# Performance work log

Hardware: AMD Instinct MI355X
Metric: run time of the kernel (lower is better)

## Reference

```python
import jax, jax.numpy as jnp
import numpy as np

TOP_K = 2


def setup_inputs() -> dict:
    key = jax.random.key(0)
    ks = jax.random.split(key, 6)
    B, S, D, F, E = 4, 2048, 1024, 4096, 8
    sd = 1.0 / np.sqrt(D)
    sf = 1.0 / np.sqrt(F)
    return {
        "x": jax.random.normal(ks[0], (B, S, D), dtype=jnp.float32),
        "gate_w": jax.random.normal(ks[1], (D, E), dtype=jnp.float32) * sd,
        "w1": jax.random.normal(ks[2], (E, D, F), dtype=jnp.float32) * sd,
        "b1": jax.random.normal(ks[3], (E, F), dtype=jnp.float32) * 0.01,
        "w2": jax.random.normal(ks[4], (E, F, D), dtype=jnp.float32) * sf,
        "b2": jax.random.normal(ks[5], (E, D), dtype=jnp.float32) * 0.01,
    }


def reference(x, gate_w, w1, b1, w2, b2):
    B, S, D = x.shape
    E = gate_w.shape[1]
    xf = x.reshape(-1, D)                        # [T, D], T = B*S
    T = xf.shape[0]

    # Gating: top-k logits, softmax over the selected k (in fp32, as in torch)
    logits = xf @ gate_w                         # [T, E]
    top_vals, top_idx = jax.lax.top_k(logits, TOP_K)            # [T, K]
    wts = jax.nn.softmax(top_vals.astype(jnp.float32), axis=-1).astype(x.dtype)

    # Dense combine weights: combine[t, e] = sum_k wts[t,k] * [top_idx[t,k]==e]
    rows = jnp.arange(T)[:, None]
    combine = jnp.zeros((T, E), dtype=x.dtype).at[rows, top_idx].add(wts)

    # Expert FFNs (dropout is identity in eval; torch GELU default = exact erf)
    out = jnp.zeros_like(xf)
    for e in range(E):
        h = jax.nn.gelu(xf @ w1[e] + b1[e], approximate=False)  # [T, F]
        out = out + combine[:, e:e + 1] * (h @ w2[e] + b2[e])
    return out.reshape(B, S, D)
```

## Files before the change

kernel.cpp:

```cpp
#include <hip/hip_runtime.h>


#define T_TOK 8192
#define D_DIM 1024
#define F_DIM 4096
#define E_NUM 8
#define BM 256
#define BN 256
#define BK 32
#define NK1 (D_DIM / BK)
#define NK2 (F_DIM / BK)
#define NX1 (F_DIM / BN)
#define NX2 (D_DIM / BN)
#define MAX_TILES (T_TOK * 2 / BM + E_NUM)

typedef float f32x4 __attribute__((ext_vector_type(4)));
typedef short bf16x8 __attribute__((ext_vector_type(8)));

__device__ __forceinline__ unsigned short f2bf(float f) {
  union { float f; unsigned u; } v; v.f = f;
  unsigned r = v.u + 0x7FFFu + ((v.u >> 16) & 1u);
  return (unsigned short)(r >> 16);
}

__device__ __forceinline__ void async_cp16(const unsigned short* g, unsigned short* l) {
  __builtin_amdgcn_global_load_lds((__attribute__((address_space(1))) void*)g,
                                   (__attribute__((address_space(3))) void*)l,
                                   16, 0, 0);
}

#define WAIT_VM4 asm volatile("s_waitcnt vmcnt(4)" ::: "memory")
#define WAIT_LGKM0 asm volatile("s_waitcnt lgkmcnt(0)" ::: "memory")
#define RAW_BARRIER asm volatile("s_barrier" ::: "memory")


__global__ void cast_x_kernel(const float* __restrict__ src,
                              unsigned short* __restrict__ dst, int n4) {
  int i = blockIdx.x * blockDim.x + threadIdx.x;
  if (i >= n4) return;
  float4 v = ((const float4*)src)[i];
  ushort4 o;
  o.x = f2bf(v.x); o.y = f2bf(v.y); o.z = f2bf(v.z); o.w = f2bf(v.w);
  ((ushort4*)dst)[i] = o;
}

__global__ __launch_bounds__(256) void transpose_cast_kernel(
    const float* __restrict__ src, unsigned short* __restrict__ dst,
    int R, int C) {
  __shared__ float tile[64][65];
  int e = blockIdx.z;
  src += (size_t)e * R * C;
  dst += (size_t)e * R * C;
  int c0 = blockIdx.x * 64;
  int r0 = blockIdx.y * 64;
  int t = threadIdx.x;
  int cl = (t & 15) * 4, rl = t >> 4;
#pragma unroll
  for (int i = 0; i < 4; ++i) {
    int r = rl + i * 16;
    float4 v = *(const float4*)(src + (size_t)(r0 + r) * C + c0 + cl);
    tile[r][cl + 0] = v.x;
    tile[r][cl + 1] = v.y;
    tile[r][cl + 2] = v.z;
    tile[r][cl + 3] = v.w;
  }
  __syncthreads();
  int rl2 = (t & 15) * 4, cl2 = t >> 4;
#pragma unroll
  for (int i = 0; i < 4; ++i) {
    int c = cl2 + i * 16;
    ushort4 o;
    o.x = f2bf(tile[rl2 + 0][c]);
    o.y = f2bf(tile[rl2 + 1][c]);
    o.z = f2bf(tile[rl2 + 2][c]);
    o.w = f2bf(tile[rl2 + 3][c]);
    *(ushort4*)(dst + (size_t)(c0 + c) * R + r0 + rl2) = o;
  }
}

__global__ __launch_bounds__(256) void gate_kernel(
    const float* __restrict__ x, const float* __restrict__ gw,
    float* __restrict__ topk_w, int* __restrict__ topk_e) {
  int t = (blockIdx.x * 256 + threadIdx.x) >> 6;
  int lane = threadIdx.x & 63;
  const float* xr = x + (size_t)t * D_DIM;
  float acc[8];
#pragma unroll
  for (int e = 0; e < 8; ++e) acc[e] = 0.f;
  for (int j = 0; j < D_DIM / 64; ++j) {
    int d = lane + 64 * j;
    float xv = xr[d];
    float4 g0 = ((const float4*)(gw + (size_t)d * 8))[0];
    float4 g1 = ((const float4*)(gw + (size_t)d * 8))[1];
    acc[0] += xv * g0.x; acc[1] += xv * g0.y;
    acc[2] += xv * g0.z; acc[3] += xv * g0.w;
    acc[4] += xv * g1.x; acc[5] += xv * g1.y;
    acc[6] += xv * g1.z; acc[7] += xv * g1.w;
  }
#pragma unroll
  for (int off = 32; off > 0; off >>= 1) {
#pragma unroll
    for (int e = 0; e < 8; ++e) acc[e] += __shfl_xor(acc[e], off);
  }
  if (lane == 0) {
    int e0 = 0; float v0 = acc[0];
#pragma unroll
    for (int e = 1; e < 8; ++e)
      if (acc[e] > v0) { v0 = acc[e]; e0 = e; }
    int e1 = -1; float v1 = -1e30f;
#pragma unroll
    for (int e = 0; e < 8; ++e)
      if (e != e0 && acc[e] > v1) { v1 = acc[e]; e1 = e; }
    float ex = expf(v1 - v0);
    float inv = 1.f / (1.f + ex);
    topk_w[2 * t] = inv;
    topk_w[2 * t + 1] = ex * inv;
    topk_e[2 * t] = e0;
    topk_e[2 * t + 1] = e1;
  }
}

__global__ void scatter_kernel(const int* __restrict__ topk_e,
                               int* __restrict__ cnt, int* __restrict__ assign) {
  int idx = blockIdx.x * blockDim.x + threadIdx.x;
  int e = topk_e[idx];
  int pos = atomicAdd(&cnt[e], 1);
  assign[e * T_TOK + pos] = idx;
}

__global__ void tiles_kernel(const int* __restrict__ cnt,
                             int* __restrict__ ndesc, int4* __restrict__ desc) {
  if (threadIdx.x != 0) return;
  int nt = 0, hb = 0;
  for (int e = 0; e < E_NUM; ++e) {
    int c = cnt[e];
    for (int s = 0; s < c; s += BM) {
      int4 d;
      d.x = e; d.y = s; d.z = hb;
      d.w = (c - s < BM) ? (c - s) : BM;
      desc[nt++] = d;
    }
    hb += c;
  }
  *ndesc = nt;
}


__global__ __launch_bounds__(512, 2) void gemm1_kernel(
    const unsigned short* __restrict__ xb, const unsigned short* __restrict__ w1t,
    const float* __restrict__ b1, const int* __restrict__ assign,
    const int* __restrict__ ndesc, const int4* __restrict__ desc,
    unsigned short* __restrict__ H) {
  const int nwg = NX1 * MAX_TILES;
  int lin = blockIdx.y * NX1 + blockIdx.x;
  int wg = (lin & 7) * (nwg >> 3) + (lin >> 3);
  int tileid = wg / NX1;
  int n0 = (wg & (NX1 - 1)) * BN;
  if (tileid >= *ndesc) return;
  int4 dc = desc[tileid];
  int e = dc.x, start = dc.y, hbase = dc.z, mcnt = dc.w;

  __shared__ __attribute__((aligned(16))) unsigned short As[2][BM * BK];
  __shared__ __attribute__((aligned(16))) unsigned short Bs[2][BN * BK];

  int tid = threadIdx.x, lane = tid & 63, wv = tid >> 6;

  int row = tid >> 2, cc = tid & 3;
  int g = (cc - row) & 3;
  int r1 = row + 128;
  int r0c = row < mcnt ? row : (mcnt - 1);
  int r1c = r1 < mcnt ? r1 : (mcnt - 1);
  int a0 = assign[e * T_TOK + start + r0c];
  int a1 = assign[e * T_TOK + start + r1c];
  const unsigned short* gA0 = xb + (size_t)(a0 >> 1) * D_DIM + g * 8;
  const unsigned short* gA1 = xb + (size_t)(a1 >> 1) * D_DIM + g * 8;
  const unsigned short* gB0 = w1t + (size_t)(e * F_DIM + n0 + row) * D_DIM + g * 8;
  const unsigned short* gB1 = w1t + (size_t)(e * F_DIM + n0 + r1) * D_DIM + g * 8;
  int loff = wv * 512;

  int kc16 = lane >> 4, r16 = lane & 15;
  int m_off = (wv & 1) * 128, n_off = (wv >> 1) * 64;
  int aoff[8], boff[4];
#pragma unroll
  for (int i = 0; i < 8; ++i) {
    int ra = m_off + i * 16 + r16;
    aoff[i] = ra * 32 + ((kc16 + ra) & 3) * 8;
  }
#pragma unroll
  for (int j = 0; j < 4; ++j) {
    int rb = n_off + j * 16 + r16;
    boff[j] = rb * 32 + ((kc16 + rb) & 3) * 8;
  }

  f32x4 acc[8][4];
#pragma unroll
  for (int i = 0; i < 8; ++i)
#pragma unroll
    for (int j = 0; j < 4; ++j) acc[i][j] = (f32x4){0.f, 0.f, 0.f, 0.f};

  auto issue = [&](int t, int b) {
    int kc = (t < NK1 ? t : NK1 - 1) * BK;
    async_cp16(gA0 + kc, &As[b][loff]);
    async_cp16(gA1 + kc, &As[b][loff + 4096]);
    async_cp16(gB0 + kc, &Bs[b][loff]);
    async_cp16(gB1 + kc, &Bs[b][loff + 4096]);
  };
  auto step = [&](int kt, int b) {
    WAIT_VM4;
    RAW_BARRIER;
    bf16x8 af[8], bfr[4];
#pragma unroll
    for (int i = 0; i < 8; ++i) af[i] = *(const bf16x8*)(&As[b][0] + aoff[i]);
#pragma unroll
    for (int j = 0; j < 4; ++j) bfr[j] = *(const bf16x8*)(&Bs[b][0] + boff[j]);
    WAIT_LGKM0;
    RAW_BARRIER;
    issue(kt + 2, b);
#pragma unroll
    for (int i = 0; i < 8; ++i)
#pragma unroll
      for (int j = 0; j < 4; ++j)
        acc[i][j] = __builtin_amdgcn_mfma_f32_16x16x32_bf16(af[i], bfr[j], acc[i][j], 0, 0, 0);
  };

  issue(0, 0);
  issue(1, 1);
  for (int kt = 0; kt < NK1; kt += 2) { step(kt, 0); step(kt + 1, 1); }

  int col = lane & 15, rbase = (lane >> 4) * 4;
  float bias[4];
#pragma unroll
  for (int j = 0; j < 4; ++j) bias[j] = b1[e * F_DIM + n0 + n_off + j * 16 + col];
#pragma unroll
  for (int i = 0; i < 8; ++i) {
#pragma unroll
    for (int rg = 0; rg < 4; ++rg) {
      int r = m_off + i * 16 + rbase + rg;
      if (r < mcnt) {
        unsigned short* hrow = H + (size_t)(hbase + start + r) * F_DIM + n0 + n_off + col;
#pragma unroll
        for (int j = 0; j < 4; ++j) {
          float v = acc[i][j][rg] + bias[j];
          v = 0.5f * v * (1.0f + erff(v * 0.70710678118654752f));
          hrow[j * 16] = f2bf(v);
        }
      }
    }
  }
}

__global__ __launch_bounds__(512, 2) void gemm2_kernel(
    const unsigned short* __restrict__ H, const unsigned short* __restrict__ w2t,
    const float* __restrict__ b2, const int* __restrict__ assign,
    const float* __restrict__ topk_w,
    const int* __restrict__ ndesc, const int4* __restrict__ desc,
    float* __restrict__ out) {
  const int nwg = NX2 * MAX_TILES;
  int lin = blockIdx.y * NX2 + blockIdx.x;
  int wg = (lin & 7) * (nwg >> 3) + (lin >> 3);
  int tileid = wg / NX2;
  int n0 = (wg & (NX2 - 1)) * BN;
  if (tileid >= *ndesc) return;
  int4 dc = desc[tileid];
  int e = dc.x, start = dc.y, hbase = dc.z, mcnt = dc.w;

  __shared__ __attribute__((aligned(16))) unsigned short As[2][BM * BK];
  __shared__ __attribute__((aligned(16))) unsigned short Bs[2][BN * BK];

  int tid = threadIdx.x, lane = tid & 63, wv = tid >> 6;

  int row = tid >> 2, cc = tid & 3;
  int g = (cc - row) & 3;
  int r1 = row + 128;
  int r0c = row < mcnt ? row : (mcnt - 1);
  int r1c = r1 < mcnt ? r1 : (mcnt - 1);
  const unsigned short* gA0 = H + (size_t)(hbase + start + r0c) * F_DIM + g * 8;
  const unsigned short* gA1 = H + (size_t)(hbase + start + r1c) * F_DIM + g * 8;
  const unsigned short* gB0 = w2t + (size_t)(e * D_DIM + n0 + row) * F_DIM + g * 8;
  const unsigned short* gB1 = w2t + (size_t)(e * D_DIM + n0 + r1) * F_DIM + g * 8;
  int loff = wv * 512;

  int kc16 = lane >> 4, r16 = lane & 15;
  int m_off = (wv & 1) * 128, n_off = (wv >> 1) * 64;
  int aoff[8], boff[4];
#pragma unroll
  for (int i = 0; i < 8; ++i) {
    int ra = m_off + i * 16 + r16;
    aoff[i] = ra * 32 + ((kc16 + ra) & 3) * 8;
  }
#pragma unroll
  for (int j = 0; j < 4; ++j) {
    int rb = n_off + j * 16 + r16;
    boff[j] = rb * 32 + ((kc16 + rb) & 3) * 8;
  }

  f32x4 acc[8][4];
#pragma unroll
  for (int i = 0; i < 8; ++i)
#pragma unroll
    for (int j = 0; j < 4; ++j) acc[i][j] = (f32x4){0.f, 0.f, 0.f, 0.f};

  auto issue = [&](int t, int b) {
    int kc = (t < NK2 ? t : NK2 - 1) * BK;
    async_cp16(gA0 + kc, &As[b][loff]);
    async_cp16(gA1 + kc, &As[b][loff + 4096]);
    async_cp16(gB0 + kc, &Bs[b][loff]);
    async_cp16(gB1 + kc, &Bs[b][loff + 4096]);
  };
  auto step = [&](int kt, int b) {
    WAIT_VM4;
    RAW_BARRIER;
    bf16x8 af[8], bfr[4];
#pragma unroll
    for (int i = 0; i < 8; ++i) af[i] = *(const bf16x8*)(&As[b][0] + aoff[i]);
#pragma unroll
    for (int j = 0; j < 4; ++j) bfr[j] = *(const bf16x8*)(&Bs[b][0] + boff[j]);
    WAIT_LGKM0;
    RAW_BARRIER;
    issue(kt + 2, b);
#pragma unroll
    for (int i = 0; i < 8; ++i)
#pragma unroll
      for (int j = 0; j < 4; ++j)
        acc[i][j] = __builtin_amdgcn_mfma_f32_16x16x32_bf16(af[i], bfr[j], acc[i][j], 0, 0, 0);
  };

  issue(0, 0);
  issue(1, 1);
  for (int kt = 0; kt < NK2; kt += 2) { step(kt, 0); step(kt + 1, 1); }

  int col = lane & 15, rbase = (lane >> 4) * 4;
  float bias[4];
#pragma unroll
  for (int j = 0; j < 4; ++j) bias[j] = b2[e * D_DIM + n0 + n_off + j * 16 + col];
#pragma unroll
  for (int i = 0; i < 8; ++i) {
#pragma unroll
    for (int rg = 0; rg < 4; ++rg) {
      int r = m_off + i * 16 + rbase + rg;
      if (r < mcnt) {
        int a = assign[e * T_TOK + start + r];
        float wt = topk_w[a];
        float* orow = out + (size_t)(a >> 1) * D_DIM + n0 + n_off + col;
#pragma unroll
        for (int j = 0; j < 4; ++j) {
          float v = acc[i][j][rg] + bias[j];
          atomicAdd(orow + j * 16, wt * v);
        }
      }
    }
  }
}


extern "C" void kernel_launch(void* const* d_in, const int* in_sizes, int n_in,
                              void* d_out, int out_size, void* d_ws, size_t ws_size,
                              hipStream_t stream) {
  const float* x      = (const float*)d_in[0];
  const float* gate_w = (const float*)d_in[1];
  const float* w1     = (const float*)d_in[2];
  const float* b1     = (const float*)d_in[3];
  const float* w2     = (const float*)d_in[4];
  const float* b2     = (const float*)d_in[5];
  float* out = (float*)d_out;

  char* ws = (char*)d_ws;
  size_t off = 0;
  auto alloc = [&](size_t bytes) {
    char* p = ws + off;
    off = (off + bytes + 255) & ~(size_t)255;
    return p;
  };
  unsigned short* xb   = (unsigned short*)alloc((size_t)T_TOK * D_DIM * 2);
  unsigned short* w1t  = (unsigned short*)alloc((size_t)E_NUM * D_DIM * F_DIM * 2);
  unsigned short* w2t  = (unsigned short*)alloc((size_t)E_NUM * D_DIM * F_DIM * 2);
  unsigned short* Hbuf = (unsigned short*)alloc((size_t)2 * T_TOK * F_DIM * 2);
  float* topk_w = (float*)alloc((size_t)2 * T_TOK * 4);
  int* topk_e   = (int*)alloc((size_t)2 * T_TOK * 4);
  int* assign   = (int*)alloc((size_t)E_NUM * T_TOK * 4);
  int* cnt      = (int*)alloc(64);
  int* ndesc    = (int*)alloc(64);
  int4* desc    = (int4*)alloc((size_t)MAX_TILES * 16);

  hipMemsetAsync(cnt, 0, 64, stream);
  hipMemsetAsync(out, 0, (size_t)out_size * 4, stream);

  cast_x_kernel<<<(T_TOK * D_DIM / 4 + 255) / 256, 256, 0, stream>>>(
      x, xb, T_TOK * D_DIM / 4);
  transpose_cast_kernel<<<dim3(F_DIM / 64, D_DIM / 64, E_NUM), 256, 0, stream>>>(
      w1, w1t, D_DIM, F_DIM);
  transpose_cast_kernel<<<dim3(D_DIM / 64, F_DIM / 64, E_NUM), 256, 0, stream>>>(
      w2, w2t, F_DIM, D_DIM);
  gate_kernel<<<T_TOK / 4, 256, 0, stream>>>(x, gate_w, topk_w, topk_e);
  scatter_kernel<<<2 * T_TOK / 256, 256, 0, stream>>>(topk_e, cnt, assign);
  tiles_kernel<<<1, 64, 0, stream>>>(cnt, ndesc, desc);
  gemm1_kernel<<<dim3(NX1, MAX_TILES), 512, 0, stream>>>(
      xb, w1t, b1, assign, ndesc, desc, Hbuf);
  gemm2_kernel<<<dim3(NX2, MAX_TILES), 512, 0, stream>>>(
      Hbuf, w2t, b2, assign, topk_w, ndesc, desc, out);
}
```

Before: 1.002 ms.

## Double K tile to 64 and split MFMA loop into four interleaved load/compute phases

Both expert GEMMs now use a BK=64 tile held in 128KB of dynamic LDS, with an 8-way XOR-swizzled layout. Each K step is split into four phases. Every phase issues part of the next tiles' async global-to-LDS loads, then runs a quarter of the MFMAs at raised wave priority. The aim is to halve the number of barrier/wait rounds per K and overlap load issue with MFMA work. The cost is that 128KB of LDS per block likely leaves room for only one 512-thread block per CU, despite launch_bounds(512,2), so occupancy falls and the pipeline has to hide latency on its own.

New measurement: 935.1 us. -6.6%, faster.

```diff
diff --git a/kernel.cpp b/kernel.cpp
--- a/kernel.cpp
+++ b/kernel.cpp
@@ -7,7 +7,7 @@
 #define E_NUM 8
 #define BM 256
 #define BN 256
-#define BK 32
+#define BK 64
 #define NK1 (D_DIM / BK)
 #define NK2 (F_DIM / BK)
 #define NX1 (F_DIM / BN)
@@ -29,7 +29,7 @@
                                    16, 0, 0);
 }
 
-#define WAIT_VM4 asm volatile("s_waitcnt vmcnt(4)" ::: "memory")
+#define WAIT_VM6 asm volatile("s_waitcnt vmcnt(6)" ::: "memory")
 #define WAIT_LGKM0 asm volatile("s_waitcnt lgkmcnt(0)" ::: "memory")
 #define RAW_BARRIER asm volatile("s_barrier" ::: "memory")
 
@@ -160,72 +160,95 @@
   int4 dc = desc[tileid];
   int e = dc.x, start = dc.y, hbase = dc.z, mcnt = dc.w;
 
-  __shared__ __attribute__((aligned(16))) unsigned short As[2][BM * BK];
-  __shared__ __attribute__((aligned(16))) unsigned short Bs[2][BN * BK];
+  extern __shared__ __attribute__((aligned(16))) unsigned short smem[];
 
   int tid = threadIdx.x, lane = tid & 63, wv = tid >> 6;
 
-  int row = tid >> 2, cc = tid & 3;
-  int g = (cc - row) & 3;
-  int r1 = row + 128;
-  int r0c = row < mcnt ? row : (mcnt - 1);
-  int r1c = r1 < mcnt ? r1 : (mcnt - 1);
-  int a0 = assign[e * T_TOK + start + r0c];
-  int a1 = assign[e * T_TOK + start + r1c];
-  const unsigned short* gA0 = xb + (size_t)(a0 >> 1) * D_DIM + g * 8;
-  const unsigned short* gA1 = xb + (size_t)(a1 >> 1) * D_DIM + g * 8;
-  const unsigned short* gB0 = w1t + (size_t)(e * F_DIM + n0 + row) * D_DIM + g * 8;
-  const unsigned short* gB1 = w1t + (size_t)(e * F_DIM + n0 + r1) * D_DIM + g * 8;
-  int loff = wv * 512;
+  int drow = tid >> 3, dcc = tid & 7;
+  int g = (dcc - drow) & 7;
+  const unsigned short* gAr[4];
+  const unsigned short* gBr[4];
+#pragma unroll
+  for (int j = 0; j < 4; ++j) {
+    int r = drow + 64 * j;
+    int rc = r < mcnt ? r : (mcnt - 1);
+    int a = assign[e * T_TOK + start + rc];
+    gAr[j] = xb + (size_t)(a >> 1) * D_DIM + g * 8;
+    gBr[j] = w1t + (size_t)(e * F_DIM + n0 + r) * D_DIM + g * 8;
+  }
+  int ldst = wv * 512;
 
   int kc16 = lane >> 4, r16 = lane & 15;
   int m_off = (wv & 1) * 128, n_off = (wv >> 1) * 64;
-  int aoff[8], boff[4];
-#pragma unroll
-  for (int i = 0; i < 8; ++i) {
-    int ra = m_off + i * 16 + r16;
-    aoff[i] = ra * 32 + ((kc16 + ra) & 3) * 8;
-  }
-#pragma unroll
-  for (int j = 0; j < 4; ++j) {
-    int rb = n_off + j * 16 + r16;
-    boff[j] = rb * 32 + ((kc16 + rb) & 3) * 8;
-  }
 
   f32x4 acc[8][4];
 #pragma unroll
   for (int i = 0; i < 8; ++i)
 #pragma unroll
     for (int j = 0; j < 4; ++j) acc[i][j] = (f32x4){0.f, 0.f, 0.f, 0.f};
-
-  auto issue = [&](int t, int b) {
-    int kc = (t < NK1 ? t : NK1 - 1) * BK;
-    async_cp16(gA0 + kc, &As[b][loff]);
-    async_cp16(gA1 + kc, &As[b][loff + 4096]);
-    async_cp16(gB0 + kc, &Bs[b][loff]);
-    async_cp16(gB1 + kc, &Bs[b][loff + 4096]);
-  };
-  auto step = [&](int kt, int b) {
-    WAIT_VM4;
+  bf16x8 bfr[4][2];
+
+  auto issueA = [&](int t, int j) {
+    int kt = t < NK1 ? t : NK1 - 1;
+    async_cp16(gAr[j] + kt * 64, smem + (t & 1) * 32768 + ldst + j * 4096);
+  };
+  auto issueB = [&](int t, int j) {
+    int kt = t < NK1 ? t : NK1 - 1;
+    async_cp16(gBr[j] + kt * 64, smem + (t & 1) * 32768 + 16384 + ldst + j * 4096);
+  };
+
+  auto phase = [&](int t, int q) {
+    const unsigned short* Ab = smem + (t & 1) * 32768;
+    const unsigned short* Bb = Ab + 16384;
+    if (q == 0) {
+#pragma unroll
+      for (int j = 0; j < 4; ++j) {
+        int rb = n_off + j * 16 + r16;
+#pragma unroll
+        for (int h = 0; h < 2; ++h)
+          bfr[j][h] = *(const bf16x8*)(Bb + rb * 64 + ((h * 4 + kc16 + rb) & 7) * 8);
+      }
+    }
+    bf16x8 af[2][2];
+#pragma unroll
+    for (int m2 = 0; m2 < 2; ++m2) {
+      int ra = m_off + (2 * q + m2) * 16 + r16;
+#pragma unroll
+      for (int h = 0; h < 2; ++h)
+        af[m2][h] = *(const bf16x8*)(Ab + ra * 64 + ((h * 4 + kc16 + ra) & 7) * 8);
+    }
+    if (q == 0)      { issueA(t + 1, 1); issueA(t + 1, 3); }
+    else if (q == 1) { issueB(t + 2, 0); issueB(t + 2, 1); }
+    else if (q == 2) { issueB(t + 2, 2); issueB(t + 2, 3); }
+    else             { issueA(t + 2, 0); issueA(t + 2, 2); }
     RAW_BARRIER;
-    bf16x8 af[8], bfr[4];
-#pragma unroll
-    for (int i = 0; i < 8; ++i) af[i] = *(const bf16x8*)(&As[b][0] + aoff[i]);
-#pragma unroll
-    for (int j = 0; j < 4; ++j) bfr[j] = *(const bf16x8*)(&Bs[b][0] + boff[j]);
     WAIT_LGKM0;
+    __builtin_amdgcn_s_setprio(1);
+#pragma unroll
+    for (int h = 0; h < 2; ++h)
+#pragma unroll
+      for (int m2 = 0; m2 < 2; ++m2)
+#pragma unroll
+        for (int j = 0; j < 4; ++j)
+          acc[2 * q + m2][j] = __builtin_amdgcn_mfma_f32_16x16x32_bf16(
+              af[m2][h], bfr[j][h], acc[2 * q + m2][j], 0, 0, 0);
+    __builtin_amdgcn_s_setprio(0);
+    if (q == 3) WAIT_VM6;
     RAW_BARRIER;
-    issue(kt + 2, b);
-#pragma unroll
-    for (int i = 0; i < 8; ++i)
-#pragma unroll
-      for (int j = 0; j < 4; ++j)
-        acc[i][j] = __builtin_amdgcn_mfma_f32_16x16x32_bf16(af[i], bfr[j], acc[i][j], 0, 0, 0);
-  };
-
-  issue(0, 0);
-  issue(1, 1);
-  for (int kt = 0; kt < NK1; kt += 2) { step(kt, 0); step(kt + 1, 1); }
+  };
+
+#pragma unroll
+  for (int j = 0; j < 4; ++j) issueB(0, j);
+#pragma unroll
+  for (int j = 0; j < 4; ++j) issueA(0, j);
+  issueB(1, 0); issueB(1, 1); issueB(1, 2); issueB(1, 3);
+  issueA(1, 0); issueA(1, 2);
+  WAIT_VM6;
+  RAW_BARRIER;
+
+  for (int t = 0; t < NK1; ++t) {
+    phase(t, 0); phase(t, 1); phase(t, 2); phase(t, 3);
+  }
 
   int col = lane & 15, rbase = (lane >> 4) * 4;
   float bias[4];
@@ -264,70 +287,94 @@
   int4 dc = desc[tileid];
   int e = dc.x, start = dc.y, hbase = dc.z, mcnt = dc.w;
 
-  __shared__ __attribute__((aligned(16))) unsigned short As[2][BM * BK];
-  __shared__ __attribute__((aligned(16))) unsigned short Bs[2][BN * BK];
+  extern __shared__ __attribute__((aligned(16))) unsigned short smem[];
 
   int tid = threadIdx.x, lane = tid & 63, wv = tid >> 6;
 
-  int row = tid >> 2, cc = tid & 3;
-  int g = (cc - row) & 3;
-  int r1 = row + 128;
-  int r0c = row < mcnt ? row : (mcnt - 1);
-  int r1c = r1 < mcnt ? r1 : (mcnt - 1);
-  const unsigned short* gA0 = H + (size_t)(hbase + start + r0c) * F_DIM + g * 8;
-  const unsigned short* gA1 = H + (size_t)(hbase + start + r1c) * F_DIM + g * 8;
-  const unsigned short* gB0 = w2t + (size_t)(e * D_DIM + n0 + row) * F_DIM + g * 8;
-  const unsigned short* gB1 = w2t + (size_t)(e * D_DIM + n0 + r1) * F_DIM + g * 8;
-  int loff = wv * 512;
+  int drow = tid >> 3, dcc = tid & 7;
+  int g = (dcc - drow) & 7;
+  const unsigned short* gAr[4];
+  const unsigned short* gBr[4];
+#pragma unroll
+  for (int j = 0; j < 4; ++j) {
+    int r = drow + 64 * j;
+    int rc = r < mcnt ? r : (mcnt - 1);
+    gAr[j] = H + (size_t)(hbase + start + rc) * F_DIM + g * 8;
+    gBr[j] = w2t + (size_t)(e * D_DIM + n0 + r) * F_DIM + g * 8;
+  }
+  int ldst = wv * 512;
 
   int kc16 = lane >> 4, r16 = lane & 15;
   int m_off = (wv & 1) * 128, n_off = (wv >> 1) * 64;
-  int aoff[8], boff[4];
-#pragma unroll
-  for (int i = 0; i < 8; ++i) {
-    int ra = m_off + i * 16 + r16;
-    aoff[i] = ra * 32 + ((kc16 + ra) & 3) * 8;
-  }
-#pragma unroll
-  for (int j = 0; j < 4; ++j) {
-    int rb = n_off + j * 16 + r16;
-    boff[j] = rb * 32 + ((kc16 + rb) & 3) * 8;
-  }
 
   f32x4 acc[8][4];
 #pragma unroll
   for (int i = 0; i < 8; ++i)
 #pragma unroll
     for (int j = 0; j < 4; ++j) acc[i][j] = (f32x4){0.f, 0.f, 0.f, 0.f};
-
-  auto issue = [&](int t, int b) {
-    int kc = (t < NK2 ? t : NK2 - 1) * BK;
-    async_cp16(gA0 + kc, &As[b][loff]);
-    async_cp16(gA1 + kc, &As[b][loff + 4096]);
-    async_cp16(gB0 + kc, &Bs[b][loff]);
-    async_cp16(gB1 + kc, &Bs[b][loff + 4096]);
-  };
-  auto step = [&](int kt, int b) {
-    WAIT_VM4;
+  bf16x8 bfr[4][2];
+
+  auto issueA = [&](int t, int j) {
+    int kt = t < NK2 ? t : NK2 - 1;
+    async_cp16(gAr[j] + kt * 64, smem + (t & 1) * 32768 + ldst + j * 4096);
+  };
+  auto issueB = [&](int t, int j) {
+    int kt = t < NK2 ? t : NK2 - 1;
+    async_cp16(gBr[j] + kt * 64, smem + (t & 1) * 32768 + 16384 + ldst + j * 4096);
+  };
+
+  auto phase = [&](int t, int q) {
+    const unsigned short* Ab = smem + (t & 1) * 32768;
+    const unsigned short* Bb = Ab + 16384;
+    if (q == 0) {
+#pragma unroll
+      for (int j = 0; j < 4; ++j) {
+        int rb = n_off + j * 16 + r16;
+#pragma unroll
+        for (int h = 0; h < 2; ++h)
+          bfr[j][h] = *(const bf16x8*)(Bb + rb * 64 + ((h * 4 + kc16 + rb) & 7) * 8);
+      }
+    }
+    bf16x8 af[2][2];
+#pragma unroll
+    for (int m2 = 0; m2 < 2; ++m2) {
+      int ra = m_off + (2 * q + m2) * 16 + r16;
+#pragma unroll
+      for (int h = 0; h < 2; ++h)
+        af[m2][h] = *(const bf16x8*)(Ab + ra * 64 + ((h * 4 + kc16 + ra) & 7) * 8);
+    }
+    if (q == 0)      { issueA(t + 1, 1); issueA(t + 1, 3); }
+    else if (q == 1) { issueB(t + 2, 0); issueB(t + 2, 1); }
+    else if (q == 2) { issueB(t + 2, 2); issueB(t + 2, 3); }
+    else             { issueA(t + 2, 0); issueA(t + 2, 2); }
     RAW_BARRIER;
-    bf16x8 af[8], bfr[4];
-#pragma unroll
-    for (int i = 0; i < 8; ++i) af[i] = *(const bf16x8*)(&As[b][0] + aoff[i]);
-#pragma unroll
-    for (int j = 0; j < 4; ++j) bfr[j] = *(const bf16x8*)(&Bs[b][0] + boff[j]);
     WAIT_LGKM0;
+    __builtin_amdgcn_s_setprio(1);
+#pragma unroll
+    for (int h = 0; h < 2; ++h)
+#pragma unroll
+      for (int m2 = 0; m2 < 2; ++m2)
+#pragma unroll
+        for (int j = 0; j < 4; ++j)
+          acc[2 * q + m2][j] = __builtin_amdgcn_mfma_f32_16x16x32_bf16(
+              af[m2][h], bfr[j][h], acc[2 * q + m2][j], 0, 0, 0);
+    __builtin_amdgcn_s_setprio(0);
+    if (q == 3) WAIT_VM6;
     RAW_BARRIER;
-    issue(kt + 2, b);
-#pragma unroll
-    for (int i = 0; i < 8; ++i)
-#pragma unroll
-      for (int j = 0; j < 4; ++j)
-        acc[i][j] = __builtin_amdgcn_mfma_f32_16x16x32_bf16(af[i], bfr[j], acc[i][j], 0, 0, 0);
-  };
-
-  issue(0, 0);
-  issue(1, 1);
-  for (int kt = 0; kt < NK2; kt += 2) { step(kt, 0); step(kt + 1, 1); }
+  };
+
+#pragma unroll
+  for (int j = 0; j < 4; ++j) issueB(0, j);
+#pragma unroll
+  for (int j = 0; j < 4; ++j) issueA(0, j);
+  issueB(1, 0); issueB(1, 1); issueB(1, 2); issueB(1, 3);
+  issueA(1, 0); issueA(1, 2);
+  WAIT_VM6;
+  RAW_BARRIER;
+
+  for (int t = 0; t < NK2; ++t) {
+    phase(t, 0); phase(t, 1); phase(t, 2); phase(t, 3);
+  }
 
   int col = lane & 15, rbase = (lane >> 4) * 4;
   float bias[4];
@@ -382,6 +429,11 @@
   int* ndesc    = (int*)alloc(64);
   int4* desc    = (int4*)alloc((size_t)MAX_TILES * 16);
 
+  hipFuncSetAttribute(reinterpret_cast<const void*>(gemm1_kernel),
+                      hipFuncAttributeMaxDynamicSharedMemorySize, 131072);
+  hipFuncSetAttribute(reinterpret_cast<const void*>(gemm2_kernel),
+                      hipFuncAttributeMaxDynamicSharedMemorySize, 131072);
+
   hipMemsetAsync(cnt, 0, 64, stream);
   hipMemsetAsync(out, 0, (size_t)out_size * 4, stream);
 
@@ -394,8 +446,8 @@
   gate_kernel<<<T_TOK / 4, 256, 0, stream>>>(x, gate_w, topk_w, topk_e);
   scatter_kernel<<<2 * T_TOK / 256, 256, 0, stream>>>(topk_e, cnt, assign);
   tiles_kernel<<<1, 64, 0, stream>>>(cnt, ndesc, desc);
-  gemm1_kernel<<<dim3(NX1, MAX_TILES), 512, 0, stream>>>(
+  gemm1_kernel<<<dim3(NX1, MAX_TILES), 512, 131072, stream>>>(
       xb, w1t, b1, assign, ndesc, desc, Hbuf);
-  gemm2_kernel<<<dim3(NX2, MAX_TILES), 512, 0, stream>>>(
+  gemm2_kernel<<<dim3(NX2, MAX_TILES), 512, 131072, stream>>>(
       Hbuf, w2t, b2, assign, topk_w, ndesc, desc, out);
 }
```
